# Optimization experiments

Hardware: AMD Instinct MI355X
Metric: run time of the kernel (lower is better)

## Reference

```python
import jax, jax.numpy as jnp
import numpy as np

B, D, S, H, L = 256, 7, 32, 512, 128  # batch, tree depth, n_symbols, hidden_size, latent_size
N = 2 ** D - 1  # nodes in complete binary tree, heap order (children of i are 2i+1, 2i+2)


def _xavier(key, shape):
    lim = float(np.sqrt(6.0 / (shape[0] + shape[1])))
    return jax.random.uniform(key, shape, jnp.float32, -lim, lim)


def setup_inputs():
    key = jax.random.key(0)
    ks = jax.random.split(key, 18)
    return {
        'symbols': jax.random.randint(ks[0], (B, N), 0, S, dtype=jnp.int32),
        'eps': jax.random.normal(ks[1], (B, L), jnp.float32),
        # Encoder GRU221: gate order [r, z, n], input weights act on one-hot symbol, hidden weights on cat(h_l, h_r)
        'ewi': _xavier(ks[2], (3 * H, S)),
        'ebi': jax.random.uniform(ks[3], (3 * H,), jnp.float32, -0.05, 0.05),
        'ewh': _xavier(ks[4], (3 * H, 2 * H)),
        'ebh': jax.random.uniform(ks[5], (3 * H,), jnp.float32, -0.05, 0.05),
        'h2mu_w': _xavier(ks[6], (L, H)),
        'h2mu_b': jax.random.uniform(ks[7], (L,), jnp.float32, -0.05, 0.05),
        'h2lv_w': _xavier(ks[8], (L, H)),
        'h2lv_b': jax.random.uniform(ks[9], (L,), jnp.float32, -0.05, 0.05),
        # Decoder
        'z2h_w': _xavier(ks[10], (H, L)),
        'z2h_b': jax.random.uniform(ks[11], (H,), jnp.float32, -0.05, 0.05),
        'h2o_w': _xavier(ks[12], (S, H)),
        'h2o_b': jax.random.uniform(ks[13], (S,), jnp.float32, -0.05, 0.05),
        # Decoder GRU122: gate order [r, z, n], each gate has 2H outputs (left/right child)
        'dwi': _xavier(ks[14], (6 * H, S)),
        'dbi': jax.random.uniform(ks[15], (6 * H,), jnp.float32, -0.05, 0.05),
        'dwh': _xavier(ks[16], (6 * H, H)),
        'dbh': jax.random.uniform(ks[17], (6 * H,), jnp.float32, -0.05, 0.05),
    }


def _hvae_forward(symbols, eps, ewi, ebi, ewh, ebh, h2mu_w, h2mu_b, h2lv_w, h2lv_b,
                  z2h_w, z2h_b, h2o_w, h2o_b, dwi, dbi, dwh, dbh):
    x_all = jax.nn.one_hot(symbols, S, dtype=jnp.float32)  # [B, N, S] node targets

    # ---- Encoder: GRU221 applied bottom-up, one batched step per tree level ----
    h = jnp.zeros((B, 2 ** D, H), jnp.float32)  # (absent) children of the deepest level
    for d in range(D - 1, -1, -1):
        n_d = 2 ** d
        x = x_all[:, n_d - 1: 2 * n_d - 1]       # [B, n_d, S] level-d symbols (heap order)
        hl, hr = h[:, 0::2], h[:, 1::2]           # [B, n_d, H] left/right child hiddens
        hcat = jnp.concatenate([hl, hr], axis=-1)
        gi = x @ ewi.T + ebi                       # [B, n_d, 3H]
        gh = hcat @ ewh.T + ebh
        r = jax.nn.sigmoid(gi[..., :H] + gh[..., :H])
        zg = jax.nn.sigmoid(gi[..., H:2 * H] + gh[..., H:2 * H])
        n = jnp.tanh(gi[..., 2 * H:] + r * gh[..., 2 * H:])
        h = (1.0 - zg) * n + zg * (hl + hr) * 0.5
    root = h[:, 0]                                 # [B, H]
    mu = root @ h2mu_w.T + h2mu_b                  # [B, L]
    logvar = root @ h2lv_w.T + h2lv_b
    zlat = mu + eps * jnp.exp(0.5 * logvar)        # reparameterized sample

    # ---- Decoder: GRU122 applied top-down, one batched step per tree level ----
    hidden = (zlat @ z2h_w.T + z2h_b)[:, None, :]  # [B, 1, H] root hidden
    preds = []
    for d in range(D):
        pred = hidden @ h2o_w.T + h2o_b            # [B, 2^d, S]
        preds.append(pred)
        if d < D - 1:
            a = jax.nn.softmax(pred, axis=-1)
            gi = a @ dwi.T + dbi                    # [B, 2^d, 6H]
            gh = hidden @ dwh.T + dbh
            r = jax.nn.sigmoid(gi[..., :2 * H] + gh[..., :2 * H])
            zg = jax.nn.sigmoid(gi[..., 2 * H:4 * H] + gh[..., 2 * H:4 * H])
            n = jnp.tanh(gi[..., 4 * H:] + r * gh[..., 4 * H:])
            dh = jnp.concatenate([hidden, hidden], axis=-1)  # h.repeat(1,1,2)
            out = (1.0 - zg) * n + zg * dh          # [B, 2^d, 2H]
            # torch.split -> (left, right); interleave as next level's hiddens (heap order)
            hidden = jnp.stack([out[..., :H], out[..., H:]], axis=2).reshape(B, 2 ** (d + 1), H)
    preds = jnp.concatenate(preds, axis=1)          # [B, N, S] per-node logits, level order
    return mu, logvar, preds


def reference(symbols, eps, ewi, ebi, ewh, ebh, h2mu_w, h2mu_b, h2lv_w, h2lv_b,
              z2h_w, z2h_b, h2o_w, h2o_b, dwi, dbi, dwh, dbh):
    return _hvae_forward(symbols, eps, ewi, ebi, ewh, ebh, h2mu_w, h2mu_b, h2lv_w, h2lv_b,
                         z2h_w, z2h_b, h2o_w, h2o_b, dwi, dbi, dwh, dbh)
```

## Files before the change

kernel.cpp:

```cpp
#include <hip/hip_runtime.h>
#include <hip/hip_bf16.h>

typedef unsigned short u16;
typedef unsigned int u32;
typedef __attribute__((ext_vector_type(8))) short short8;
typedef __attribute__((ext_vector_type(4))) float f32x4;

#define WAITV(N) asm volatile("s_waitcnt vmcnt(" #N ")" ::: "memory")

__device__ __forceinline__ float sigmoidf_(float x) { return 1.0f / (1.0f + expf(-x)); }

__device__ __forceinline__ float bf2f(u16 u) {
    union { u32 i; float f; } v; v.i = ((u32)u) << 16; return v.f;
}
__device__ __forceinline__ u16 f2bf(float f) {
    union { float f; u32 i; } v; v.f = f;
    u32 lsb = (v.i >> 16) & 1u;
    v.i += 0x7fffu + lsb;
    return (u16)(v.i >> 16);
}

__device__ __forceinline__ void gload16(const u16* g, u16* l) {
    __builtin_amdgcn_global_load_lds(
        (const __attribute__((address_space(1))) u32*)g,
        (__attribute__((address_space(3))) u32*)l, 16, 0, 0);
}

__global__ __launch_bounds__(256) void prep(
    const float* __restrict__ ewh, const float* __restrict__ dwh,
    const float* __restrict__ dwi, const float* __restrict__ ewi,
    const float* __restrict__ h2o_w, const int* __restrict__ symbols,
    const float* __restrict__ ebi, const float* __restrict__ ebh,
    u16* __restrict__ ewh_b, u16* __restrict__ dwh_b, u16* __restrict__ dwi_b,
    u16* __restrict__ ewi_b, u16* __restrict__ wo_b, u16* __restrict__ oneh,
    u16* __restrict__ ltab)
{
    int idx = blockIdx.x * 256 + threadIdx.x;
    if (idx < 1572864) { ewh_b[idx] = f2bf(ewh[idx]); return; }
    idx -= 1572864;
    if (idx < 1572864) { dwh_b[idx] = f2bf(dwh[idx]); return; }
    idx -= 1572864;
    if (idx < 98304) { dwi_b[idx] = f2bf(dwi[idx]); return; }
    idx -= 98304;
    if (idx < 49152) { ewi_b[idx] = f2bf(ewi[idx]); return; }
    idx -= 49152;
    if (idx < 16384) { wo_b[idx] = f2bf(h2o_w[idx]); return; }
    idx -= 16384;
    if (idx < 1040384) {
        int col = idx & 31, row = idx >> 5;
        oneh[idx] = (col == symbols[row]) ? (u16)0x3F80 : (u16)0;
        return;
    }
    idx -= 1040384;
    if (idx < 16384) {
        int c = idx & 511, sym = idx >> 9;
        float r = sigmoidf_(ewi[c * 32 + sym]          + ebi[c]        + ebh[c]);
        float z = sigmoidf_(ewi[(512 + c) * 32 + sym]  + ebi[512 + c]  + ebh[512 + c]);
        float n = tanhf(    ewi[(1024 + c) * 32 + sym] + ebi[1024 + c] + r * ebh[1024 + c]);
        ltab[idx] = f2bf((1.0f - z) * n);
    }
}

template<int RF, bool LEAF>
__global__ __launch_bounds__(256, 2) void enc_tile(
    const u16* __restrict__ A, const u16* __restrict__ W,
    const u16* __restrict__ oneh, const u16* __restrict__ Wi,
    const u16* __restrict__ tab, const int* __restrict__ symbols,
    const float* __restrict__ ebi, const float* __restrict__ ebh,
    u16* __restrict__ hout, int dlog, int node_base)
{
    constexpr int BM = RF * 32;
    constexpr int NCA = BM / 64;
    constexpr int NS = 32;
    __shared__ alignas(16) u16 Als[4][BM * 32];
    __shared__ alignas(16) u16 Bls[4][192 * 32];
    const int tid  = threadIdx.x;
    const int lane = tid & 63;
    const int wid  = tid >> 6;
    const int wr = wid >> 1, wc = wid & 1;
    const int lr = lane & 15, lk = lane >> 4;
    const int m0 = blockIdx.x * BM;
    const int c0 = blockIdx.y * 64;
    const int mask = (1 << dlog) - 1;

    size_t a_goff[NCA]; int a_loff[NCA];
    int symL[NCA], symR[NCA];
#pragma unroll
    for (int j = 0; j < NCA; ++j) {
        int a = wid * NCA + j;
        int r_ = a * 16 + (lane >> 2);
        int kps = (lane & 3) ^ ((r_ >> 1) & 3);
        a_loff[j] = a * 512 + lane * 8;
        if constexpr (LEAF) {
            int rg = m0 + r_;
            int b_ = rg >> dlog, jj = rg & mask;
            int cbase = b_ * 127 + 2 * (node_base + jj) + 1;
            symL[j] = symbols[cbase];
            symR[j] = symbols[cbase + 1];
            a_goff[j] = kps * 8;
        } else {
            a_goff[j] = (size_t)(m0 + r_) * 1024 + kps * 8;
            symL[j] = symR[j] = 0;
        }
    }
    size_t b_goff[3]; int b_loff[3];
#pragma unroll
    for (int j = 0; j < 3; ++j) {
        int b = wid * 3 + j;
        int rr = b * 16 + (lane >> 2);
        int kps = (lane & 3) ^ ((rr >> 1) & 3);
        int grow = (rr >> 6) * 512 + c0 + (rr & 63);
        b_goff[j] = (size_t)grow * 1024 + kps * 8;
        b_loff[j] = b * 512 + lane * 8;
    }
    int a_roff[RF];
#pragma unroll
    for (int i = 0; i < RF; ++i) {
        int row = wr * (RF * 16) + i * 16 + lr;
        a_roff[i] = row * 32 + (lk ^ ((row >> 1) & 3)) * 8;
    }
    int b_roff[3][2];
#pragma unroll
    for (int s = 0; s < 3; ++s)
#pragma unroll
        for (int cf = 0; cf < 2; ++cf) {
            int row = s * 64 + wc * 32 + cf * 16 + lr;
            b_roff[s][cf] = row * 32 + (lk ^ ((row >> 1) & 3)) * 8;
        }

    f32x4 acc[4][2][RF];
#pragma unroll
    for (int s = 0; s < 4; ++s)
#pragma unroll
        for (int cf = 0; cf < 2; ++cf)
#pragma unroll
            for (int i = 0; i < RF; ++i) acc[s][cf][i] = (f32x4){0.f, 0.f, 0.f, 0.f};

    auto issue = [&](int stg) {
        const int buf = stg & 3;
        const int nk = stg * 32;
#pragma unroll
        for (int j = 0; j < NCA; ++j) {
            if constexpr (LEAF) {
                const u16* src = (nk < 512)
                    ? tab + (size_t)symL[j] * 512 + nk + a_goff[j]
                    : tab + (size_t)symR[j] * 512 + (nk - 512) + a_goff[j];
                gload16(src, &Als[buf][a_loff[j]]);
            } else {
                gload16(A + a_goff[j] + nk, &Als[buf][a_loff[j]]);
            }
        }
#pragma unroll
        for (int j = 0; j < 3; ++j) gload16(W + b_goff[j] + nk, &Bls[buf][b_loff[j]]);
    };
    auto compute = [&](int buf) {
        short8 a[RF];
#pragma unroll
        for (int i = 0; i < RF; ++i)
            a[i] = *reinterpret_cast<const short8*>(&Als[buf][a_roff[i]]);
#pragma unroll
        for (int s = 0; s < 3; ++s)
#pragma unroll
            for (int cf = 0; cf < 2; ++cf) {
                short8 b = *reinterpret_cast<const short8*>(&Bls[buf][b_roff[s][cf]]);
#pragma unroll
                for (int i = 0; i < RF; ++i)
                    acc[s][cf][i] = __builtin_amdgcn_mfma_f32_16x16x32_bf16(a[i], b, acc[s][cf][i], 0, 0, 0);
            }
    };

    issue(0); issue(1); issue(2);
    for (int t = 0; t < NS - 2; ++t) {
        if constexpr (RF == 4) WAITV(10); else WAITV(8);
        __builtin_amdgcn_s_barrier();
        if (t + 3 < NS) issue(t + 3);
        compute(t & 3);
    }
    if constexpr (RF == 4) WAITV(5); else WAITV(4);
    __builtin_amdgcn_s_barrier();
    compute((NS - 2) & 3);
    WAITV(0);
    __builtin_amdgcn_s_barrier();
    compute((NS - 1) & 3);

    {
        short8 oh[RF];
#pragma unroll
        for (int i = 0; i < RF; ++i) {
            int m = m0 + wr * (RF * 16) + i * 16 + lr;
            int b_ = m >> dlog, j_ = m & mask;
            oh[i] = *reinterpret_cast<const short8*>(
                oneh + (size_t)(b_ * 127 + node_base + j_) * 32 + lk * 8);
        }
#pragma unroll
        for (int s = 0; s < 3; ++s) {
            const int d = (s == 2) ? 3 : s;
#pragma unroll
            for (int cf = 0; cf < 2; ++cf) {
                short8 wb = *reinterpret_cast<const short8*>(
                    Wi + (size_t)(s * 512 + c0 + wc * 32 + cf * 16 + lr) * 32 + lk * 8);
#pragma unroll
                for (int i = 0; i < RF; ++i)
                    acc[d][cf][i] = __builtin_amdgcn_mfma_f32_16x16x32_bf16(oh[i], wb, acc[d][cf][i], 0, 0, 0);
            }
        }
    }

    float ebr[2], ebz[2], ebin[2], ebhn[2];
#pragma unroll
    for (int cf = 0; cf < 2; ++cf) {
        int c = c0 + wc * 32 + cf * 16 + lr;
        ebr[cf]  = ebi[c] + ebh[c];
        ebz[cf]  = ebi[512 + c] + ebh[512 + c];
        ebin[cf] = ebi[1024 + c];
        ebhn[cf] = ebh[1024 + c];
    }
#pragma unroll
    for (int i = 0; i < RF; ++i)
#pragma unroll
        for (int r = 0; r < 4; ++r) {
            int m = m0 + wr * (RF * 16) + i * 16 + lk * 4 + r;
            int symLm = 0, symRm = 0;
            if constexpr (LEAF) {
                int b_ = m >> dlog, jj = m & mask;
                int cbase = b_ * 127 + 2 * (node_base + jj) + 1;
                symLm = symbols[cbase];
                symRm = symbols[cbase + 1];
            }
#pragma unroll
            for (int cf = 0; cf < 2; ++cf) {
                int c = c0 + wc * 32 + cf * 16 + lr;
                float rr_ = sigmoidf_(acc[0][cf][i][r] + ebr[cf]);
                float zz  = sigmoidf_(acc[1][cf][i][r] + ebz[cf]);
                float nn  = tanhf(acc[3][cf][i][r] + ebin[cf] + rr_ * (acc[2][cf][i][r] + ebhn[cf]));
                float hl, hr;
                if constexpr (LEAF) {
                    hl = bf2f(tab[(size_t)symLm * 512 + c]);
                    hr = bf2f(tab[(size_t)symRm * 512 + c]);
                } else {
                    hl = bf2f(A[(size_t)m * 1024 + c]);
                    hr = bf2f(A[(size_t)m * 1024 + 512 + c]);
                }
                hout[(size_t)m * 512 + c] = f2bf((1.0f - zz) * nn + zz * (hl + hr) * 0.5f);
            }
        }
}

__global__ __launch_bounds__(256) void mid1(
    const u16* __restrict__ root, const float* __restrict__ h2mu_w,
    const float* __restrict__ h2mu_b, const float* __restrict__ h2lv_w,
    const float* __restrict__ h2lv_b, const float* __restrict__ eps,
    float* __restrict__ zlat, float* __restrict__ out_mu,
    float* __restrict__ out_lv)
{
    int b = blockIdx.x, t = threadIdx.x;
    __shared__ float rs[512];
    rs[t]       = bf2f(root[(size_t)b * 512 + t]);
    rs[t + 256] = bf2f(root[(size_t)b * 512 + t + 256]);
    __syncthreads();
    const float* w = (t < 128) ? (h2mu_w + (size_t)t * 512) : (h2lv_w + (size_t)(t - 128) * 512);
    float acc = 0.0f;
    for (int k = 0; k < 512; ++k) acc += rs[k] * w[k];
    acc += (t < 128) ? h2mu_b[t] : h2lv_b[t - 128];
    __shared__ float vals[256];
    vals[t] = acc;
    __syncthreads();
    if (t < 128) {
        float mu = vals[t], lv = vals[t + 128];
        float zl = mu + eps[b * 128 + t] * expf(0.5f * lv);
        zlat[b * 128 + t] = zl;
        out_mu[b * 128 + t] = mu;
        out_lv[b * 128 + t] = lv;
    }
}

__global__ __launch_bounds__(512) void mid2(
    const float* __restrict__ zlat, const float* __restrict__ z2h_w,
    const float* __restrict__ z2h_b, u16* __restrict__ hidden)
{
    int b = blockIdx.x, t = threadIdx.x;
    __shared__ float zs[128];
    if (t < 128) zs[t] = zlat[b * 128 + t];
    __syncthreads();
    float acc = z2h_b[t];
    for (int k = 0; k < 128; ++k) acc += zs[k] * z2h_w[(size_t)t * 128 + k];
    hidden[(size_t)b * 512 + t] = f2bf(acc);
}

__global__ __launch_bounds__(256) void pred_mfma(
    const u16* __restrict__ hidden, const u16* __restrict__ Wo,
    const float* __restrict__ h2o_b, u16* __restrict__ aout,
    float* __restrict__ preds_out, int dlog, int node_base, int write_a)
{
    const int lane = threadIdx.x & 63;
    const int wid  = threadIdx.x >> 6;
    const int lr = lane & 15, lk = lane >> 4;
    const int m0 = blockIdx.x * 64 + wid * 16;

    f32x4 acc0 = (f32x4){0.f, 0.f, 0.f, 0.f};
    f32x4 acc1 = (f32x4){0.f, 0.f, 0.f, 0.f};
    const u16* Arow = hidden + (size_t)(m0 + lr) * 512 + lk * 8;
    const u16* B0 = Wo + (size_t)lr * 512 + lk * 8;
    const u16* B1 = Wo + (size_t)(16 + lr) * 512 + lk * 8;
#pragma unroll
    for (int k0 = 0; k0 < 512; k0 += 32) {
        short8 a  = *reinterpret_cast<const short8*>(Arow + k0);
        short8 b0 = *reinterpret_cast<const short8*>(B0 + k0);
        short8 b1 = *reinterpret_cast<const short8*>(B1 + k0);
        acc0 = __builtin_amdgcn_mfma_f32_16x16x32_bf16(a, b0, acc0, 0, 0, 0);
        acc1 = __builtin_amdgcn_mfma_f32_16x16x32_bf16(a, b1, acc1, 0, 0, 0);
    }
    const float bb0 = h2o_b[lr], bb1 = h2o_b[16 + lr];
    const int dmask = (1 << dlog) - 1;
#pragma unroll
    for (int r = 0; r < 4; ++r) {
        float p0 = acc0[r] + bb0;
        float p1 = acc1[r] + bb1;
        float mx = fmaxf(p0, p1);
#pragma unroll
        for (int off = 1; off < 16; off <<= 1) mx = fmaxf(mx, __shfl_xor(mx, off));
        float e0 = expf(p0 - mx), e1 = expf(p1 - mx);
        float s = e0 + e1;
#pragma unroll
        for (int off = 1; off < 16; off <<= 1) s += __shfl_xor(s, off);
        int m = m0 + lk * 4 + r;
        int b_ = m >> dlog, j_ = m & dmask;
        size_t o = (size_t)(b_ * 127 + node_base + j_) * 32;
        preds_out[o + lr] = p0;
        preds_out[o + 16 + lr] = p1;
        if (write_a) {
            float inv = 1.0f / s;
            aout[(size_t)m * 32 + lr]      = f2bf(e0 * inv);
            aout[(size_t)m * 32 + 16 + lr] = f2bf(e1 * inv);
        }
    }
}

template<int RF>
__global__ __launch_bounds__(256, 2) void dec_tile(
    const u16* __restrict__ Hin, const u16* __restrict__ aB,
    const u16* __restrict__ Wh, const u16* __restrict__ Wi,
    const float* __restrict__ dbh, const float* __restrict__ dbi,
    u16* __restrict__ Hout)
{
    constexpr int BM = RF * 32;
    constexpr int NCA = BM / 64;
    constexpr int NS = 16;
    __shared__ alignas(16) u16 Als[4][BM * 32];
    __shared__ alignas(16) u16 Bls[4][192 * 32];
    const int tid  = threadIdx.x;
    const int lane = tid & 63;
    const int wid  = tid >> 6;
    const int wr = wid >> 1, wc = wid & 1;
    const int lr = lane & 15, lk = lane >> 4;
    const int m0 = blockIdx.x * BM;
    const int c0 = blockIdx.y * 64;

    size_t a_goff[NCA]; int a_loff[NCA];
#pragma unroll
    for (int j = 0; j < NCA; ++j) {
        int a = wid * NCA + j;
        int r_ = a * 16 + (lane >> 2);
        int kps = (lane & 3) ^ ((r_ >> 1) & 3);
        a_goff[j] = (size_t)(m0 + r_) * 512 + kps * 8;
        a_loff[j] = a * 512 + lane * 8;
    }
    size_t b_goff[3]; int b_loff[3];
#pragma unroll
    for (int j = 0; j < 3; ++j) {
        int b = wid * 3 + j;
        int rr = b * 16 + (lane >> 2);
        int kps = (lane & 3) ^ ((rr >> 1) & 3);
        int grow = (rr >> 6) * 1024 + c0 + (rr & 63);
        b_goff[j] = (size_t)grow * 512 + kps * 8;
        b_loff[j] = b * 512 + lane * 8;
    }
    int a_roff[RF];
#pragma unroll
    for (int i = 0; i < RF; ++i) {
        int row = wr * (RF * 16) + i * 16 + lr;
        a_roff[i] = row * 32 + (lk ^ ((row >> 1) & 3)) * 8;
    }
    int b_roff[3][2];
#pragma unroll
    for (int s = 0; s < 3; ++s)
#pragma unroll
        for (int cf = 0; cf < 2; ++cf) {
            int row = s * 64 + wc * 32 + cf * 16 + lr;
            b_roff[s][cf] = row * 32 + (lk ^ ((row >> 1) & 3)) * 8;
        }

    f32x4 acc[4][2][RF];
#pragma unroll
    for (int s = 0; s < 4; ++s)
#pragma unroll
        for (int cf = 0; cf < 2; ++cf)
#pragma unroll
            for (int i = 0; i < RF; ++i) acc[s][cf][i] = (f32x4){0.f, 0.f, 0.f, 0.f};

    auto issue = [&](int stg) {
        const int buf = stg & 3;
        const int nk = stg * 32;
#pragma unroll
        for (int j = 0; j < NCA; ++j) gload16(Hin + a_goff[j] + nk, &Als[buf][a_loff[j]]);
#pragma unroll
        for (int j = 0; j < 3; ++j) gload16(Wh + b_goff[j] + nk, &Bls[buf][b_loff[j]]);
    };
    auto compute = [&](int buf) {
        short8 a[RF];
#pragma unroll
        for (int i = 0; i < RF; ++i)
            a[i] = *reinterpret_cast<const short8*>(&Als[buf][a_roff[i]]);
#pragma unroll
        for (int s = 0; s < 3; ++s)
#pragma unroll
            for (int cf = 0; cf < 2; ++cf) {
                short8 b = *reinterpret_cast<const short8*>(&Bls[buf][b_roff[s][cf]]);
#pragma unroll
                for (int i = 0; i < RF; ++i)
                    acc[s][cf][i] = __builtin_amdgcn_mfma_f32_16x16x32_bf16(a[i], b, acc[s][cf][i], 0, 0, 0);
            }
    };

    issue(0); issue(1); issue(2);
    for (int t = 0; t < NS - 2; ++t) {
        if constexpr (RF == 4) WAITV(10); else WAITV(8);
        __builtin_amdgcn_s_barrier();
        if (t + 3 < NS) issue(t + 3);
        compute(t & 3);
    }
    if constexpr (RF == 4) WAITV(5); else WAITV(4);
    __builtin_amdgcn_s_barrier();
    compute((NS - 2) & 3);
    WAITV(0);
    __builtin_amdgcn_s_barrier();
    compute((NS - 1) & 3);

#pragma unroll
    for (int i = 0; i < RF; ++i) {
        short8 aw = *reinterpret_cast<const short8*>(
            aB + (size_t)(m0 + wr * (RF * 16) + i * 16 + lr) * 32 + lk * 8);
#pragma unroll
        for (int s = 0; s < 3; ++s) {
            const int d = (s == 2) ? 3 : s;
#pragma unroll
            for (int cf = 0; cf < 2; ++cf) {
                short8 b = *reinterpret_cast<const short8*>(
                    Wi + (size_t)(s * 1024 + c0 + wc * 32 + cf * 16 + lr) * 32 + lk * 8);
                acc[d][cf][i] = __builtin_amdgcn_mfma_f32_16x16x32_bf16(aw, b, acc[d][cf][i], 0, 0, 0);
            }
        }
    }

#pragma unroll
    for (int i = 0; i < RF; ++i)
#pragma unroll
        for (int r = 0; r < 4; ++r) {
            int m = m0 + wr * (RF * 16) + i * 16 + lk * 4 + r;
#pragma unroll
            for (int cf = 0; cf < 2; ++cf) {
                int c = c0 + wc * 32 + cf * 16 + lr;
                float rr_ = sigmoidf_(acc[0][cf][i][r] + dbh[c]        + dbi[c]);
                float zz  = sigmoidf_(acc[1][cf][i][r] + dbh[1024 + c] + dbi[1024 + c]);
                float nn  = tanhf(acc[3][cf][i][r] + dbi[2048 + c] + rr_ * (acc[2][cf][i][r] + dbh[2048 + c]));
                float hid = bf2f(Hin[(size_t)m * 512 + (c & 511)]);
                Hout[(size_t)m * 1024 + c] = f2bf((1.0f - zz) * nn + zz * hid);
            }
        }
}

extern "C" void kernel_launch(void* const* d_in, const int* in_sizes, int n_in,
                              void* d_out, int out_size, void* d_ws, size_t ws_size,
                              hipStream_t stream) {
    const int*   symbols = (const int*)  d_in[0];
    const float* eps     = (const float*)d_in[1];
    const float* ewi     = (const float*)d_in[2];
    const float* ebi     = (const float*)d_in[3];
    const float* ewh     = (const float*)d_in[4];
    const float* ebh     = (const float*)d_in[5];
    const float* h2mu_w  = (const float*)d_in[6];
    const float* h2mu_b  = (const float*)d_in[7];
    const float* h2lv_w  = (const float*)d_in[8];
    const float* h2lv_b  = (const float*)d_in[9];
    const float* z2h_w   = (const float*)d_in[10];
    const float* z2h_b   = (const float*)d_in[11];
    const float* h2o_w   = (const float*)d_in[12];
    const float* h2o_b   = (const float*)d_in[13];
    const float* dwi     = (const float*)d_in[14];
    const float* dbi     = (const float*)d_in[15];
    const float* dwh     = (const float*)d_in[16];
    const float* dbh     = (const float*)d_in[17];

    float* out    = (float*)d_out;
    float* out_mu = out;
    float* out_lv = out + 256 * 128;
    float* out_pr = out + 2 * 256 * 128;

    u16* bufL  = (u16*)d_ws;
    u16* bufS  = bufL  + (size_t)16384 * 512;
    u16* ewh_b = bufS  + (size_t)8192 * 512;
    u16* dwh_b = ewh_b + (size_t)1536 * 1024;
    u16* dwi_b = dwh_b + (size_t)3072 * 512;
    u16* ewi_b = dwi_b + (size_t)3072 * 32;
    u16* wo_b  = ewi_b + (size_t)1536 * 32;
    u16* ltab  = wo_b  + (size_t)32 * 512;
    u16* oneh  = ltab  + (size_t)32 * 512;
    u16* aBuf  = oneh  + (size_t)32512 * 32;
    float* zlat = (float*)(aBuf + (size_t)8192 * 32);

    prep<<<(4366336 + 255) / 256, 256, 0, stream>>>(
        ewh, dwh, dwi, ewi, h2o_w, symbols, ebi, ebh,
        ewh_b, dwh_b, dwi_b, ewi_b, wo_b, oneh, ltab);

    enc_tile<4, true><<<dim3(64, 8), 256, 0, stream>>>(
        nullptr, ewh_b, oneh, ewi_b, ltab, symbols, ebi, ebh, bufS, 5, 31);
    const u16* src = bufS;
    u16*       dst = bufL;
    for (int d = 4; d >= 0; --d) {
        int M = 256 << d;
        enc_tile<2, false><<<dim3(M / 64, 8), 256, 0, stream>>>(
            src, ewh_b, oneh, ewi_b, ltab, symbols, ebi, ebh, dst, d, (1 << d) - 1);
        const u16* t = src; src = dst; dst = (u16*)t;
    }
    mid1<<<256, 256, 0, stream>>>(src, h2mu_w, h2mu_b, h2lv_w, h2lv_b, eps, zlat, out_mu, out_lv);
    mid2<<<256, 512, 0, stream>>>(zlat, z2h_w, z2h_b, bufL);

    const u16* hsrc = bufL;
    u16*       hdst = bufS;
    for (int d = 0; d < 6; ++d) {
        int M = 256 << d;
        pred_mfma<<<M / 64, 256, 0, stream>>>(hsrc, wo_b, h2o_b, aBuf, out_pr, d, (1 << d) - 1, 1);
        if (M >= 8192)
            dec_tile<4><<<dim3(M / 128, 16), 256, 0, stream>>>(hsrc, aBuf, dwh_b, dwi_b, dbh, dbi, hdst);
        else
            dec_tile<2><<<dim3(M / 64, 16), 256, 0, stream>>>(hsrc, aBuf, dwh_b, dwi_b, dbh, dbi, hdst);
        const u16* t = hsrc; hsrc = hdst; hdst = (u16*)t;
    }
    pred_mfma<<<16384 / 64, 256, 0, stream>>>(hsrc, wo_b, h2o_b, aBuf, out_pr, 6, 63, 0);
}
```

Measured before the change: 393.7 us.

## Transpose MFMA operands for vectorized epilogue stores and use fast transcendentals

Swaps the A/B operands of every MFMA so that each lane's accumulator holds four consecutive output columns of one row rather than four rows of one column. The GRU and softmax epilogues are rewritten to load biases and hidden values as float4/ushort4 and to write outputs as packed 8-byte stores instead of scalar 2-byte stores. The softmax reduction needs fewer cross-lane shuffles as a result. Sigmoid, tanh and reciprocal are replaced with __expf/rcp-based approximations, which trades a little accuracy for fewer instructions in the epilogue.

```diff
diff --git a/kernel.cpp b/kernel.cpp
--- a/kernel.cpp
+++ b/kernel.cpp
@@ -9,6 +9,14 @@
 #define WAITV(N) asm volatile("s_waitcnt vmcnt(" #N ")" ::: "memory")
 
 __device__ __forceinline__ float sigmoidf_(float x) { return 1.0f / (1.0f + expf(-x)); }
+__device__ __forceinline__ float fsig(float x) {
+    return __builtin_amdgcn_rcpf(1.0f + __expf(-x));
+}
+__device__ __forceinline__ float ftanh(float x) {
+    x = fminf(fmaxf(x, -15.0f), 15.0f);
+    float t = __expf(2.0f * x);
+    return (t - 1.0f) * __builtin_amdgcn_rcpf(t + 1.0f);
+}
 
 __device__ __forceinline__ float bf2f(u16 u) {
     union { u32 i; float f; } v; v.i = ((u32)u) << 16; return v.f;
@@ -165,7 +173,7 @@
                 short8 b = *reinterpret_cast<const short8*>(&Bls[buf][b_roff[s][cf]]);
 #pragma unroll
                 for (int i = 0; i < RF; ++i)
-                    acc[s][cf][i] = __builtin_amdgcn_mfma_f32_16x16x32_bf16(a[i], b, acc[s][cf][i], 0, 0, 0);
+                    acc[s][cf][i] = __builtin_amdgcn_mfma_f32_16x16x32_bf16(b, a[i], acc[s][cf][i], 0, 0, 0);
             }
     };
 
@@ -201,49 +209,64 @@
                     Wi + (size_t)(s * 512 + c0 + wc * 32 + cf * 16 + lr) * 32 + lk * 8);
 #pragma unroll
                 for (int i = 0; i < RF; ++i)
-                    acc[d][cf][i] = __builtin_amdgcn_mfma_f32_16x16x32_bf16(oh[i], wb, acc[d][cf][i], 0, 0, 0);
-            }
-        }
-    }
-
-    float ebr[2], ebz[2], ebin[2], ebhn[2];
+                    acc[d][cf][i] = __builtin_amdgcn_mfma_f32_16x16x32_bf16(wb, oh[i], acc[d][cf][i], 0, 0, 0);
+            }
+        }
+    }
+
+    float4 ebr4[2], ebz4[2], ebin4[2], ebhn4[2];
+    int cb[2];
 #pragma unroll
     for (int cf = 0; cf < 2; ++cf) {
-        int c = c0 + wc * 32 + cf * 16 + lr;
-        ebr[cf]  = ebi[c] + ebh[c];
-        ebz[cf]  = ebi[512 + c] + ebh[512 + c];
-        ebin[cf] = ebi[1024 + c];
-        ebhn[cf] = ebh[1024 + c];
-    }
-#pragma unroll
-    for (int i = 0; i < RF; ++i)
-#pragma unroll
-        for (int r = 0; r < 4; ++r) {
-            int m = m0 + wr * (RF * 16) + i * 16 + lk * 4 + r;
-            int symLm = 0, symRm = 0;
+        cb[cf] = c0 + wc * 32 + cf * 16 + lk * 4;
+        float4 bi0 = *reinterpret_cast<const float4*>(ebi + cb[cf]);
+        float4 bh0 = *reinterpret_cast<const float4*>(ebh + cb[cf]);
+        float4 bi1 = *reinterpret_cast<const float4*>(ebi + 512 + cb[cf]);
+        float4 bh1 = *reinterpret_cast<const float4*>(ebh + 512 + cb[cf]);
+        ebr4[cf] = make_float4(bi0.x + bh0.x, bi0.y + bh0.y, bi0.z + bh0.z, bi0.w + bh0.w);
+        ebz4[cf] = make_float4(bi1.x + bh1.x, bi1.y + bh1.y, bi1.z + bh1.z, bi1.w + bh1.w);
+        ebin4[cf] = *reinterpret_cast<const float4*>(ebi + 1024 + cb[cf]);
+        ebhn4[cf] = *reinterpret_cast<const float4*>(ebh + 1024 + cb[cf]);
+    }
+#pragma unroll
+    for (int i = 0; i < RF; ++i) {
+        int m = m0 + wr * (RF * 16) + i * 16 + lr;
+        int symLm = 0, symRm = 0;
+        if constexpr (LEAF) {
+            int b_ = m >> dlog, jj = m & mask;
+            int cbase_ = b_ * 127 + 2 * (node_base + jj) + 1;
+            symLm = symbols[cbase_];
+            symRm = symbols[cbase_ + 1];
+        }
+#pragma unroll
+        for (int cf = 0; cf < 2; ++cf) {
+            ushort4 hl4, hr4;
             if constexpr (LEAF) {
-                int b_ = m >> dlog, jj = m & mask;
-                int cbase = b_ * 127 + 2 * (node_base + jj) + 1;
-                symLm = symbols[cbase];
-                symRm = symbols[cbase + 1];
-            }
-#pragma unroll
-            for (int cf = 0; cf < 2; ++cf) {
-                int c = c0 + wc * 32 + cf * 16 + lr;
-                float rr_ = sigmoidf_(acc[0][cf][i][r] + ebr[cf]);
-                float zz  = sigmoidf_(acc[1][cf][i][r] + ebz[cf]);
-                float nn  = tanhf(acc[3][cf][i][r] + ebin[cf] + rr_ * (acc[2][cf][i][r] + ebhn[cf]));
-                float hl, hr;
-                if constexpr (LEAF) {
-                    hl = bf2f(tab[(size_t)symLm * 512 + c]);
-                    hr = bf2f(tab[(size_t)symRm * 512 + c]);
-                } else {
-                    hl = bf2f(A[(size_t)m * 1024 + c]);
-                    hr = bf2f(A[(size_t)m * 1024 + 512 + c]);
-                }
-                hout[(size_t)m * 512 + c] = f2bf((1.0f - zz) * nn + zz * (hl + hr) * 0.5f);
-            }
-        }
+                hl4 = *reinterpret_cast<const ushort4*>(tab + (size_t)symLm * 512 + cb[cf]);
+                hr4 = *reinterpret_cast<const ushort4*>(tab + (size_t)symRm * 512 + cb[cf]);
+            } else {
+                hl4 = *reinterpret_cast<const ushort4*>(A + (size_t)m * 1024 + cb[cf]);
+                hr4 = *reinterpret_cast<const ushort4*>(A + (size_t)m * 1024 + 512 + cb[cf]);
+            }
+            const float eb_r[4] = {ebr4[cf].x, ebr4[cf].y, ebr4[cf].z, ebr4[cf].w};
+            const float eb_z[4] = {ebz4[cf].x, ebz4[cf].y, ebz4[cf].z, ebz4[cf].w};
+            const float eb_in[4] = {ebin4[cf].x, ebin4[cf].y, ebin4[cf].z, ebin4[cf].w};
+            const float eb_hn[4] = {ebhn4[cf].x, ebhn4[cf].y, ebhn4[cf].z, ebhn4[cf].w};
+            const u16 hlv[4] = {hl4.x, hl4.y, hl4.z, hl4.w};
+            const u16 hrv[4] = {hr4.x, hr4.y, hr4.z, hr4.w};
+            ushort4 outv;
+            u16* ov = reinterpret_cast<u16*>(&outv);
+#pragma unroll
+            for (int r = 0; r < 4; ++r) {
+                float rr_ = fsig(acc[0][cf][i][r] + eb_r[r]);
+                float zz  = fsig(acc[1][cf][i][r] + eb_z[r]);
+                float nn  = ftanh(acc[3][cf][i][r] + eb_in[r] + rr_ * (acc[2][cf][i][r] + eb_hn[r]));
+                float hm = (bf2f(hlv[r]) + bf2f(hrv[r])) * 0.5f;
+                ov[r] = f2bf((1.0f - zz) * nn + zz * hm);
+            }
+            *reinterpret_cast<ushort4*>(hout + (size_t)m * 512 + cb[cf]) = outv;
+        }
+    }
 }
 
 __global__ __launch_bounds__(256) void mid1(
@@ -307,32 +330,38 @@
         short8 a  = *reinterpret_cast<const short8*>(Arow + k0);
         short8 b0 = *reinterpret_cast<const short8*>(B0 + k0);
         short8 b1 = *reinterpret_cast<const short8*>(B1 + k0);
-        acc0 = __builtin_amdgcn_mfma_f32_16x16x32_bf16(a, b0, acc0, 0, 0, 0);
-        acc1 = __builtin_amdgcn_mfma_f32_16x16x32_bf16(a, b1, acc1, 0, 0, 0);
-    }
-    const float bb0 = h2o_b[lr], bb1 = h2o_b[16 + lr];
-    const int dmask = (1 << dlog) - 1;
-#pragma unroll
-    for (int r = 0; r < 4; ++r) {
-        float p0 = acc0[r] + bb0;
-        float p1 = acc1[r] + bb1;
-        float mx = fmaxf(p0, p1);
-#pragma unroll
-        for (int off = 1; off < 16; off <<= 1) mx = fmaxf(mx, __shfl_xor(mx, off));
-        float e0 = expf(p0 - mx), e1 = expf(p1 - mx);
-        float s = e0 + e1;
-#pragma unroll
-        for (int off = 1; off < 16; off <<= 1) s += __shfl_xor(s, off);
-        int m = m0 + lk * 4 + r;
-        int b_ = m >> dlog, j_ = m & dmask;
-        size_t o = (size_t)(b_ * 127 + node_base + j_) * 32;
-        preds_out[o + lr] = p0;
-        preds_out[o + 16 + lr] = p1;
-        if (write_a) {
-            float inv = 1.0f / s;
-            aout[(size_t)m * 32 + lr]      = f2bf(e0 * inv);
-            aout[(size_t)m * 32 + 16 + lr] = f2bf(e1 * inv);
-        }
+        acc0 = __builtin_amdgcn_mfma_f32_16x16x32_bf16(b0, a, acc0, 0, 0, 0);
+        acc1 = __builtin_amdgcn_mfma_f32_16x16x32_bf16(b1, a, acc1, 0, 0, 0);
+    }
+    float4 bb0 = *reinterpret_cast<const float4*>(h2o_b + lk * 4);
+    float4 bb1 = *reinterpret_cast<const float4*>(h2o_b + 16 + lk * 4);
+    float p0[4], p1[4];
+    p0[0] = acc0[0] + bb0.x; p0[1] = acc0[1] + bb0.y; p0[2] = acc0[2] + bb0.z; p0[3] = acc0[3] + bb0.w;
+    p1[0] = acc1[0] + bb1.x; p1[1] = acc1[1] + bb1.y; p1[2] = acc1[2] + bb1.z; p1[3] = acc1[3] + bb1.w;
+    float mx = fmaxf(fmaxf(fmaxf(p0[0], p0[1]), fmaxf(p0[2], p0[3])),
+                     fmaxf(fmaxf(p1[0], p1[1]), fmaxf(p1[2], p1[3])));
+    mx = fmaxf(mx, __shfl_xor(mx, 16));
+    mx = fmaxf(mx, __shfl_xor(mx, 32));
+    float e0[4], e1[4], s = 0.0f;
+#pragma unroll
+    for (int r = 0; r < 4; ++r) { e0[r] = __expf(p0[r] - mx); e1[r] = __expf(p1[r] - mx); s += e0[r] + e1[r]; }
+    s += __shfl_xor(s, 16);
+    s += __shfl_xor(s, 32);
+
+    int m = m0 + lr;
+    int b_ = m >> dlog, j_ = m & ((1 << dlog) - 1);
+    size_t o = (size_t)(b_ * 127 + node_base + j_) * 32;
+    *reinterpret_cast<float4*>(preds_out + o + lk * 4)      = make_float4(p0[0], p0[1], p0[2], p0[3]);
+    *reinterpret_cast<float4*>(preds_out + o + 16 + lk * 4) = make_float4(p1[0], p1[1], p1[2], p1[3]);
+    if (write_a) {
+        float inv = __builtin_amdgcn_rcpf(s);
+        ushort4 a0, a1;
+        u16* av0 = reinterpret_cast<u16*>(&a0);
+        u16* av1 = reinterpret_cast<u16*>(&a1);
+#pragma unroll
+        for (int r = 0; r < 4; ++r) { av0[r] = f2bf(e0[r] * inv); av1[r] = f2bf(e1[r] * inv); }
+        *reinterpret_cast<ushort4*>(aout + (size_t)m * 32 + lk * 4)      = a0;
+        *reinterpret_cast<ushort4*>(aout + (size_t)m * 32 + 16 + lk * 4) = a1;
     }
 }
 
@@ -418,7 +447,7 @@
                 short8 b = *reinterpret_cast<const short8*>(&Bls[buf][b_roff[s][cf]]);
 #pragma unroll
                 for (int i = 0; i < RF; ++i)
-                    acc[s][cf][i] = __builtin_amdgcn_mfma_f32_16x16x32_bf16(a[i], b, acc[s][cf][i], 0, 0, 0);
+                    acc[s][cf][i] = __builtin_amdgcn_mfma_f32_16x16x32_bf16(b, a[i], acc[s][cf][i], 0, 0, 0);
             }
     };
 
@@ -447,26 +476,48 @@
             for (int cf = 0; cf < 2; ++cf) {
                 short8 b = *reinterpret_cast<const short8*>(
                     Wi + (size_t)(s * 1024 + c0 + wc * 32 + cf * 16 + lr) * 32 + lk * 8);
-                acc[d][cf][i] = __builtin_amdgcn_mfma_f32_16x16x32_bf16(aw, b, acc[d][cf][i], 0, 0, 0);
-            }
-        }
-    }
-
-#pragma unroll
-    for (int i = 0; i < RF; ++i)
-#pragma unroll
-        for (int r = 0; r < 4; ++r) {
-            int m = m0 + wr * (RF * 16) + i * 16 + lk * 4 + r;
-#pragma unroll
-            for (int cf = 0; cf < 2; ++cf) {
-                int c = c0 + wc * 32 + cf * 16 + lr;
-                float rr_ = sigmoidf_(acc[0][cf][i][r] + dbh[c]        + dbi[c]);
-                float zz  = sigmoidf_(acc[1][cf][i][r] + dbh[1024 + c] + dbi[1024 + c]);
-                float nn  = tanhf(acc[3][cf][i][r] + dbi[2048 + c] + rr_ * (acc[2][cf][i][r] + dbh[2048 + c]));
-                float hid = bf2f(Hin[(size_t)m * 512 + (c & 511)]);
-                Hout[(size_t)m * 1024 + c] = f2bf((1.0f - zz) * nn + zz * hid);
-            }
-        }
+                acc[d][cf][i] = __builtin_amdgcn_mfma_f32_16x16x32_bf16(b, aw, acc[d][cf][i], 0, 0, 0);
+            }
+        }
+    }
+
+    float4 br4[2], bz4[2], bin4[2], bhn4[2];
+    int cb[2];
+#pragma unroll
+    for (int cf = 0; cf < 2; ++cf) {
+        cb[cf] = c0 + wc * 32 + cf * 16 + lk * 4;
+        float4 h0 = *reinterpret_cast<const float4*>(dbh + cb[cf]);
+        float4 i0 = *reinterpret_cast<const float4*>(dbi + cb[cf]);
+        float4 h1 = *reinterpret_cast<const float4*>(dbh + 1024 + cb[cf]);
+        float4 i1 = *reinterpret_cast<const float4*>(dbi + 1024 + cb[cf]);
+        br4[cf] = make_float4(h0.x + i0.x, h0.y + i0.y, h0.z + i0.z, h0.w + i0.w);
+        bz4[cf] = make_float4(h1.x + i1.x, h1.y + i1.y, h1.z + i1.z, h1.w + i1.w);
+        bin4[cf] = *reinterpret_cast<const float4*>(dbi + 2048 + cb[cf]);
+        bhn4[cf] = *reinterpret_cast<const float4*>(dbh + 2048 + cb[cf]);
+    }
+#pragma unroll
+    for (int i = 0; i < RF; ++i) {
+        int m = m0 + wr * (RF * 16) + i * 16 + lr;
+#pragma unroll
+        for (int cf = 0; cf < 2; ++cf) {
+            ushort4 hid4 = *reinterpret_cast<const ushort4*>(Hin + (size_t)m * 512 + (cb[cf] & 511));
+            const float b_r[4] = {br4[cf].x, br4[cf].y, br4[cf].z, br4[cf].w};
+            const float b_z[4] = {bz4[cf].x, bz4[cf].y, bz4[cf].z, bz4[cf].w};
+            const float b_in[4] = {bin4[cf].x, bin4[cf].y, bin4[cf].z, bin4[cf].w};
+            const float b_hn[4] = {bhn4[cf].x, bhn4[cf].y, bhn4[cf].z, bhn4[cf].w};
+            const u16 hv[4] = {hid4.x, hid4.y, hid4.z, hid4.w};
+            ushort4 outv;
+            u16* ov = reinterpret_cast<u16*>(&outv);
+#pragma unroll
+            for (int r = 0; r < 4; ++r) {
+                float rr_ = fsig(acc[0][cf][i][r] + b_r[r]);
+                float zz  = fsig(acc[1][cf][i][r] + b_z[r]);
+                float nn  = ftanh(acc[3][cf][i][r] + b_in[r] + rr_ * (acc[2][cf][i][r] + b_hn[r]));
+                ov[r] = f2bf((1.0f - zz) * nn + zz * bf2f(hv[r]));
+            }
+            *reinterpret_cast<ushort4*>(Hout + (size_t)m * 1024 + cb[cf]) = outv;
+        }
+    }
 }
 
 extern "C" void kernel_launch(void* const* d_in, const int* in_sizes, int n_in,
```

After: 349.8 us. 11.2% less time.
